# Kernel tuning notes

Hardware: AMD Instinct MI355X
Metric: run time of the kernel (lower is better)

Reference implementation:

```python
import jax, jax.numpy as jnp
import numpy as np

BS = 4            # block_size
QMAX = 255.0      # 2**8 - 1 for both weights and activations; qmin = 0


def _fake_quant(v, scale, zero):
    # round/clamp/dequant exactly as the torch module
    q = jnp.clip(jnp.round(v / scale + zero), 0.0, QMAX)
    return (q - zero) * scale


def setup_inputs() -> dict:
    key = jax.random.key(0)
    k1, k2, k3 = jax.random.split(key, 3)
    B, IN, OUT = 1024, 4096, 4096
    nb = IN // BS  # num_blocks_in_fea = 1024
    x = jax.random.normal(k1, (B, IN), jnp.float32)
    weight = jax.random.normal(k2, (OUT, IN), jnp.float32) * 0.02
    bias = jax.random.normal(k3, (OUT,), jnp.float32) * 0.01
    # --- calibrate_weight (vectorized): per [out_idx, block] min/max ---
    wb = weight.reshape(OUT, nb, BS)
    wmin, wmax = wb.min(-1), wb.max(-1)
    valid = wmax > wmin
    w_scales = jnp.where(valid, (wmax - wmin) / QMAX, 1.0)
    w_zeros = jnp.where(valid, -wmin / w_scales, 0.0)  # qmin=0 -> zero = -min/scale
    # --- calibrate_activation (vectorized): per-block min/max over all rows ---
    xb = x.reshape(B, nb, BS)
    amin, amax = xb.min(axis=(0, 2)), xb.max(axis=(0, 2))
    avalid = amax > amin
    a_scales = jnp.where(avalid, (amax - amin) / QMAX, 1.0)
    a_zeros = jnp.where(avalid, -amin / a_scales, 0.0)
    return {"x": x, "weight": weight, "bias": bias,
            "w_scales": w_scales, "w_zeros": w_zeros,
            "a_scales": a_scales, "a_zeros": a_zeros}


def reference(x, weight, bias, w_scales, w_zeros, a_scales, a_zeros):
    # mode == 'fake_quant': quantize activations and weights per block, then linear
    B, IN = x.shape
    OUT = weight.shape[0]
    nb = IN // BS
    xq = _fake_quant(x.reshape(B, nb, BS),
                     a_scales[None, :, None], a_zeros[None, :, None]).reshape(B, IN)
    wq = _fake_quant(weight.reshape(OUT, nb, BS),
                     w_scales[:, :, None], w_zeros[:, :, None]).reshape(OUT, IN)
    return xq @ wq.T + bias
```

## Files before the change

### kernel.cpp

```cpp
#include <hip/hip_runtime.h>
#include <hip/hip_bf16.h>
#include <stdint.h>

#define DI __device__ __forceinline__

typedef float f32x4 __attribute__((ext_vector_type(4)));
typedef __bf16 bf16x8 __attribute__((ext_vector_type(8)));

static constexpr int M = 1024;
static constexpr int N = 4096;
static constexpr int K = 4096;

DI unsigned short f2bf(float f) {
  union { __hip_bfloat16 h; unsigned short u; } cv;
  cv.h = __float2bfloat16(f);
  return cv.u;
}

__global__ __launch_bounds__(256) void fq_kernel(
    const float* __restrict__ x, const float* __restrict__ wt,
    const float* __restrict__ a_scales, const float* __restrict__ a_zeros,
    const float* __restrict__ w_scales, const float* __restrict__ w_zeros,
    unsigned short* __restrict__ xq, unsigned short* __restrict__ wq) {
  constexpr int n4x = M * K / 4;
  constexpr int n4w = N * K / 4;
  const int stride = gridDim.x * blockDim.x;
  for (int t = blockIdx.x * blockDim.x + threadIdx.x; t < n4x + n4w; t += stride) {
    float s, z;
    const float4* src;
    unsigned short* dst;
    int idx;
    if (t < n4x) {
      idx = t;
      const int si = t & (K / 4 - 1);
      s = a_scales[si]; z = a_zeros[si];
      src = reinterpret_cast<const float4*>(x);
      dst = xq;
    } else {
      idx = t - n4x;
      s = w_scales[idx]; z = w_zeros[idx];
      src = reinterpret_cast<const float4*>(wt);
      dst = wq;
    }
    const float rs = 1.0f / s;
    const float4 v = src[idx];
    ushort4 o;
    float q;
    q = rintf(fmaf(v.x, rs, z)); q = fminf(fmaxf(q, 0.0f), 255.0f); o.x = f2bf((q - z) * s);
    q = rintf(fmaf(v.y, rs, z)); q = fminf(fmaxf(q, 0.0f), 255.0f); o.y = f2bf((q - z) * s);
    q = rintf(fmaf(v.z, rs, z)); q = fminf(fmaxf(q, 0.0f), 255.0f); o.z = f2bf((q - z) * s);
    q = rintf(fmaf(v.w, rs, z)); q = fminf(fmaxf(q, 0.0f), 255.0f); o.w = f2bf((q - z) * s);
    reinterpret_cast<ushort4*>(dst)[idx] = o;
  }
}

static constexpr int BM = 128, BN = 128, BK = 64;
static constexpr int KT = K / BK;

DI void gl2lds16(const void* g, void* l) {
  __builtin_amdgcn_global_load_lds(
      (const __attribute__((address_space(1))) void*)g,
      (__attribute__((address_space(3))) void*)l, 16, 0, 0);
}

__global__ __launch_bounds__(512) void gemm_kernel(
    const unsigned short* __restrict__ Aq,
    const unsigned short* __restrict__ Bq,
    const float* __restrict__ bias,
    float* __restrict__ C) {
  __shared__ char smem[98304];

  const int tid  = threadIdx.x;
  const int lane = tid & 63;
  const int w    = tid >> 6;
  const int kh   = w >> 2;
  const int wq4  = w & 3;
  const int wm   = (wq4 >> 1) * 64;
  const int wn   = (wq4 & 1) * 64;
  const int fr   = lane & 15;

  const int xcd = blockIdx.x & 7;
  const int j   = blockIdx.x >> 3;
  const int bm  = (j & 7) * BM;
  const int bn  = (xcd * 4 + (j >> 3)) * BN;

  const int lrow = lane >> 3;
  const int scol = ((lane & 7) ^ lrow) * 8;
  const unsigned short* gA0 = Aq + (size_t)(bm +      8 * w + lrow) * K + scol;
  const unsigned short* gA1 = Aq + (size_t)(bm + 64 + 8 * w + lrow) * K + scol;
  const unsigned short* gB0 = Bq + (size_t)(bn +      8 * w + lrow) * K + scol;
  const unsigned short* gB1 = Bq + (size_t)(bn + 64 + 8 * w + lrow) * K + scol;
  const int wofs = w * 1024;

  auto stage = [&](int k0, int s) {
    char* base = smem + s * 32768;
    gl2lds16(gA0 + k0, base + wofs);
    gl2lds16(gA1 + k0, base + 8192 + wofs);
    gl2lds16(gB0 + k0, base + 16384 + wofs);
    gl2lds16(gB1 + k0, base + 24576 + wofs);
  };

  const int slot = kh * 4 + (lane >> 4);
  int aoff[4], boff[4];
#pragma unroll
  for (int f = 0; f < 4; ++f) {
    const int ra = wm + f * 16 + fr;
    aoff[f] = ra * 64 + (slot ^ (ra & 7)) * 8;
    const int rb = wn + f * 16 + fr;
    boff[f] = rb * 64 + (slot ^ (rb & 7)) * 8;
  }

  f32x4 acc[4][4] = {};

  auto compute = [&](int s) {
    const unsigned short* As = (const unsigned short*)(smem + s * 32768);
    const unsigned short* Bs = As + 8192;
    bf16x8 aF[4], bF[4];
#pragma unroll
    for (int f = 0; f < 4; ++f) aF[f] = *(const bf16x8*)(As + aoff[f]);
#pragma unroll
    for (int f = 0; f < 4; ++f) bF[f] = *(const bf16x8*)(Bs + boff[f]);
#pragma unroll
    for (int fm = 0; fm < 4; ++fm)
#pragma unroll
      for (int fn = 0; fn < 4; ++fn)
        acc[fm][fn] = __builtin_amdgcn_mfma_f32_16x16x32_bf16(aF[fm], bF[fn], acc[fm][fn], 0, 0, 0);
  };

#define BAR() do { __builtin_amdgcn_sched_barrier(0); \
                   __builtin_amdgcn_s_barrier(); \
                   __builtin_amdgcn_sched_barrier(0); } while (0)

  stage(0, 0);
  stage(BK, 1);

  int cur = 0, nxt = 2;
  for (int t = 0; t < KT; ++t) {
    if (t + 2 < KT) {
      stage((t + 2) * BK, nxt);
      asm volatile("s_waitcnt vmcnt(8)" ::: "memory");
    } else if (t + 1 < KT) {
      asm volatile("s_waitcnt vmcnt(4)" ::: "memory");
    } else {
      asm volatile("s_waitcnt vmcnt(0)" ::: "memory");
    }
    BAR();
    compute(cur);
    BAR();
    cur = (cur == 2) ? 0 : cur + 1;
    nxt = (nxt == 2) ? 0 : nxt + 1;
  }
#undef BAR

  __syncthreads();
  float* cb = (float*)smem;
  if (kh == 1) {
#pragma unroll
    for (int fm = 0; fm < 4; ++fm)
#pragma unroll
      for (int fn = 0; fn < 4; ++fn) {
        const int sl = (fm * 4 + fn) ^ (lane & 15);
        *(f32x4*)(cb + ((wq4 * 64 + lane) * 16 + sl) * 4) = acc[fm][fn];
      }
  }
  __syncthreads();
  if (kh == 0) {
#pragma unroll
    for (int fm = 0; fm < 4; ++fm) {
#pragma unroll
      for (int fn = 0; fn < 4; ++fn) {
        const int sl = (fm * 4 + fn) ^ (lane & 15);
        f32x4 o = *(const f32x4*)(cb + ((wq4 * 64 + lane) * 16 + sl) * 4);
        o += acc[fm][fn];
        const int col = bn + wn + fn * 16 + fr;
        const float bv = bias[col];
        const int r0 = bm + wm + fm * 16 + ((lane >> 4) << 2);
#pragma unroll
        for (int r = 0; r < 4; ++r)
          C[(size_t)(r0 + r) * N + col] = o[r] + bv;
      }
    }
  }
}

extern "C" void kernel_launch(void* const* d_in, const int* in_sizes, int n_in,
                              void* d_out, int out_size, void* d_ws, size_t ws_size,
                              hipStream_t stream) {
  const float* x        = (const float*)d_in[0];
  const float* weight   = (const float*)d_in[1];
  const float* bias     = (const float*)d_in[2];
  const float* w_scales = (const float*)d_in[3];
  const float* w_zeros  = (const float*)d_in[4];
  const float* a_scales = (const float*)d_in[5];
  const float* a_zeros  = (const float*)d_in[6];
  float* out = (float*)d_out;

  unsigned short* xq = (unsigned short*)d_ws;
  unsigned short* wq = xq + (size_t)M * K;

  fq_kernel<<<2048, 256, 0, stream>>>(x, weight, a_scales, a_zeros,
                                      w_scales, w_zeros, xq, wq);
  gemm_kernel<<<(M / BM) * (N / BN), 512, 0, stream>>>(xq, wq, bias, out);
}
```

Before: 193.4 us.

## Pre-pack activations in MFMA fragment order and load A directly to registers

The quantize kernel now writes the activation matrix in a fragment-packed layout matching the MFMA operand order, so the GEMM reads A straight from global memory into registers, prefetching one k-step ahead, instead of staging it through LDS. Only B goes through the LDS triple buffer, which halves shared memory use and removes one barrier per k-step. The cost is uncoalesced-looking strided reads of x in the quantize pass, A tiles re-read from global/L2 by every block without LDS sharing, and more register pressure from double-buffered A fragments.

```diff
diff --git a/kernel.cpp b/kernel.cpp
--- a/kernel.cpp
+++ b/kernel.cpp
@@ -6,6 +6,7 @@
 
 typedef float f32x4 __attribute__((ext_vector_type(4)));
 typedef __bf16 bf16x8 __attribute__((ext_vector_type(8)));
+typedef unsigned short ushort8v __attribute__((ext_vector_type(8)));
 
 static constexpr int M = 1024;
 static constexpr int N = 4096;
@@ -17,40 +18,52 @@
   return cv.u;
 }
 
+DI unsigned short fq1(float v, float s, float rs, float z) {
+  float q = rintf(fmaf(v, rs, z));
+  q = fminf(fmaxf(q, 0.0f), 255.0f);
+  return f2bf((q - z) * s);
+}
+
+static constexpr int NXP = M * K / 8;
+static constexpr int N4W = N * K / 4;
+
 __global__ __launch_bounds__(256) void fq_kernel(
     const float* __restrict__ x, const float* __restrict__ wt,
     const float* __restrict__ a_scales, const float* __restrict__ a_zeros,
     const float* __restrict__ w_scales, const float* __restrict__ w_zeros,
-    unsigned short* __restrict__ xq, unsigned short* __restrict__ wq) {
-  constexpr int n4x = M * K / 4;
-  constexpr int n4w = N * K / 4;
+    unsigned short* __restrict__ xqp, unsigned short* __restrict__ wq) {
   const int stride = gridDim.x * blockDim.x;
-  for (int t = blockIdx.x * blockDim.x + threadIdx.x; t < n4x + n4w; t += stride) {
-    float s, z;
-    const float4* src;
-    unsigned short* dst;
-    int idx;
-    if (t < n4x) {
-      idx = t;
-      const int si = t & (K / 4 - 1);
-      s = a_scales[si]; z = a_zeros[si];
-      src = reinterpret_cast<const float4*>(x);
-      dst = xq;
+  for (int v = blockIdx.x * blockDim.x + threadIdx.x; v < NXP + N4W; v += stride) {
+    if (v < NXP) {
+      const int p   = v;
+      const int fr  = p & 15;
+      const int ks  = (p >> 4) & 3;
+      const int rt  = (p >> 6) & 63;
+      const int khh = (p >> 12) & 1;
+      const int tk  = p >> 13;
+      const int row = rt * 16 + fr;
+      const int col = tk * 64 + khh * 32 + ks * 8;
+      const float* src = x + (size_t)row * K + col;
+      const float4 v0 = *(const float4*)src;
+      const float4 v1 = *(const float4*)(src + 4);
+      const int si = col >> 2;
+      const float s0 = a_scales[si],     z0 = a_zeros[si],     rs0 = 1.0f / s0;
+      const float s1 = a_scales[si + 1], z1 = a_zeros[si + 1], rs1 = 1.0f / s1;
+      ushort8v o;
+      o[0] = fq1(v0.x, s0, rs0, z0); o[1] = fq1(v0.y, s0, rs0, z0);
+      o[2] = fq1(v0.z, s0, rs0, z0); o[3] = fq1(v0.w, s0, rs0, z0);
+      o[4] = fq1(v1.x, s1, rs1, z1); o[5] = fq1(v1.y, s1, rs1, z1);
+      o[6] = fq1(v1.z, s1, rs1, z1); o[7] = fq1(v1.w, s1, rs1, z1);
+      *(ushort8v*)(xqp + (size_t)p * 8) = o;
     } else {
-      idx = t - n4x;
-      s = w_scales[idx]; z = w_zeros[idx];
-      src = reinterpret_cast<const float4*>(wt);
-      dst = wq;
-    }
-    const float rs = 1.0f / s;
-    const float4 v = src[idx];
-    ushort4 o;
-    float q;
-    q = rintf(fmaf(v.x, rs, z)); q = fminf(fmaxf(q, 0.0f), 255.0f); o.x = f2bf((q - z) * s);
-    q = rintf(fmaf(v.y, rs, z)); q = fminf(fmaxf(q, 0.0f), 255.0f); o.y = f2bf((q - z) * s);
-    q = rintf(fmaf(v.z, rs, z)); q = fminf(fmaxf(q, 0.0f), 255.0f); o.z = f2bf((q - z) * s);
-    q = rintf(fmaf(v.w, rs, z)); q = fminf(fmaxf(q, 0.0f), 255.0f); o.w = f2bf((q - z) * s);
-    reinterpret_cast<ushort4*>(dst)[idx] = o;
+      const int q = v - NXP;
+      const float s = w_scales[q], z = w_zeros[q], rs = 1.0f / s;
+      const float4 t4 = reinterpret_cast<const float4*>(wt)[q];
+      ushort4 o;
+      o.x = fq1(t4.x, s, rs, z); o.y = fq1(t4.y, s, rs, z);
+      o.z = fq1(t4.z, s, rs, z); o.w = fq1(t4.w, s, rs, z);
+      reinterpret_cast<ushort4*>(wq)[q] = o;
+    }
   }
 }
 
@@ -64,11 +77,11 @@
 }
 
 __global__ __launch_bounds__(512) void gemm_kernel(
-    const unsigned short* __restrict__ Aq,
+    const unsigned short* __restrict__ Ap,
     const unsigned short* __restrict__ Bq,
     const float* __restrict__ bias,
     float* __restrict__ C) {
-  __shared__ char smem[98304];
+  __shared__ char smem[65536];
 
   const int tid  = threadIdx.x;
   const int lane = tid & 63;
@@ -86,71 +99,70 @@
 
   const int lrow = lane >> 3;
   const int scol = ((lane & 7) ^ lrow) * 8;
-  const unsigned short* gA0 = Aq + (size_t)(bm +      8 * w + lrow) * K + scol;
-  const unsigned short* gA1 = Aq + (size_t)(bm + 64 + 8 * w + lrow) * K + scol;
   const unsigned short* gB0 = Bq + (size_t)(bn +      8 * w + lrow) * K + scol;
   const unsigned short* gB1 = Bq + (size_t)(bn + 64 + 8 * w + lrow) * K + scol;
   const int wofs = w * 1024;
 
   auto stage = [&](int k0, int s) {
-    char* base = smem + s * 32768;
-    gl2lds16(gA0 + k0, base + wofs);
-    gl2lds16(gA1 + k0, base + 8192 + wofs);
-    gl2lds16(gB0 + k0, base + 16384 + wofs);
-    gl2lds16(gB1 + k0, base + 24576 + wofs);
+    char* base = smem + s * 16384;
+    gl2lds16(gB0 + k0, base + wofs);
+    gl2lds16(gB1 + k0, base + 8192 + wofs);
   };
 
   const int slot = kh * 4 + (lane >> 4);
-  int aoff[4], boff[4];
+  int boff[4];
 #pragma unroll
   for (int f = 0; f < 4; ++f) {
-    const int ra = wm + f * 16 + fr;
-    aoff[f] = ra * 64 + (slot ^ (ra & 7)) * 8;
     const int rb = wn + f * 16 + fr;
     boff[f] = rb * 64 + (slot ^ (rb & 7)) * 8;
   }
 
+  const unsigned short* aBase = Ap + (size_t)kh * 32768 +
+                                ((bm + wm) >> 4) * 512 +
+                                (lane >> 4) * 128 + (lane & 15) * 8;
+
   f32x4 acc[4][4] = {};
-
-  auto compute = [&](int s) {
-    const unsigned short* As = (const unsigned short*)(smem + s * 32768);
-    const unsigned short* Bs = As + 8192;
-    bf16x8 aF[4], bF[4];
-#pragma unroll
-    for (int f = 0; f < 4; ++f) aF[f] = *(const bf16x8*)(As + aoff[f]);
+  bf16x8 aA[4], aB[4];
+  int cur = 0;
+
+  auto body = [&](int t, bf16x8 (&aCur)[4], bf16x8 (&aNxt)[4]) {
+    if (t < KT - 1) asm volatile("s_waitcnt vmcnt(6)" ::: "memory");
+    else            asm volatile("s_waitcnt vmcnt(4)" ::: "memory");
+    __builtin_amdgcn_sched_barrier(0);
+    __builtin_amdgcn_s_barrier();
+    __builtin_amdgcn_sched_barrier(0);
+    if (t + 2 < KT) {
+      int nb = cur + 2; if (nb >= 3) nb -= 3;
+      stage((t + 2) * BK, nb);
+    }
+    if (t + 1 < KT) {
+      const unsigned short* ap = aBase + (size_t)(t + 1) * 65536;
+#pragma unroll
+      for (int fm = 0; fm < 4; ++fm)
+        aNxt[fm] = *(const bf16x8*)(ap + fm * 512);
+    }
+    const unsigned short* Bs = (const unsigned short*)(smem + cur * 16384);
+    bf16x8 bF[4];
 #pragma unroll
     for (int f = 0; f < 4; ++f) bF[f] = *(const bf16x8*)(Bs + boff[f]);
 #pragma unroll
     for (int fm = 0; fm < 4; ++fm)
 #pragma unroll
       for (int fn = 0; fn < 4; ++fn)
-        acc[fm][fn] = __builtin_amdgcn_mfma_f32_16x16x32_bf16(aF[fm], bF[fn], acc[fm][fn], 0, 0, 0);
+        acc[fm][fn] = __builtin_amdgcn_mfma_f32_16x16x32_bf16(aCur[fm], bF[fn], acc[fm][fn], 0, 0, 0);
+    cur = (cur + 1 == 3) ? 0 : cur + 1;
   };
-
-#define BAR() do { __builtin_amdgcn_sched_barrier(0); \
-                   __builtin_amdgcn_s_barrier(); \
-                   __builtin_amdgcn_sched_barrier(0); } while (0)
 
   stage(0, 0);
   stage(BK, 1);
-
-  int cur = 0, nxt = 2;
-  for (int t = 0; t < KT; ++t) {
-    if (t + 2 < KT) {
-      stage((t + 2) * BK, nxt);
-      asm volatile("s_waitcnt vmcnt(8)" ::: "memory");
-    } else if (t + 1 < KT) {
-      asm volatile("s_waitcnt vmcnt(4)" ::: "memory");
-    } else {
-      asm volatile("s_waitcnt vmcnt(0)" ::: "memory");
-    }
-    BAR();
-    compute(cur);
-    BAR();
-    cur = (cur == 2) ? 0 : cur + 1;
-    nxt = (nxt == 2) ? 0 : nxt + 1;
-  }
-#undef BAR
+#pragma unroll
+  for (int fm = 0; fm < 4; ++fm)
+    aA[fm] = *(const bf16x8*)(aBase + fm * 512);
+
+  for (int t = 0; t < KT; t += 2) {
+    body(t,     aA, aB);
+    body(t + 1, aB, aA);
+  }
 
   __syncthreads();
   float* cb = (float*)smem;
@@ -195,10 +207,10 @@
   const float* a_zeros  = (const float*)d_in[6];
   float* out = (float*)d_out;
 
-  unsigned short* xq = (unsigned short*)d_ws;
-  unsigned short* wq = xq + (size_t)M * K;
+  unsigned short* xqp = (unsigned short*)d_ws;
+  unsigned short* wq  = xqp + (size_t)M * K;
 
   fq_kernel<<<2048, 256, 0, stream>>>(x, weight, a_scales, a_zeros,
-                                      w_scales, w_zeros, xq, wq);
-  gemm_kernel<<<(M / BM) * (N / BN), 512, 0, stream>>>(xq, wq, bias, out);
-}
+                                      w_scales, w_zeros, xqp, wq);
+  gemm_kernel<<<(M / BM) * (N / BN), 512, 0, stream>>>(xqp, wq, bias, out);
+}
```

New measurement: 207.0 us. 1.07x slower.
